# Performance work log

Measured on AMD Instinct MI355X. Metric: run time of the kernel, lower is better.

## Reference

```python
import math
import jax, jax.numpy as jnp
import numpy as np

SCALE = 4; K = 7; R = 3; K2 = K * K
BANDS = 10; FEAT = 64; HID = 256; HEADS = 4
LH = 96; LW = 96; H = LH * SCALE; W = LW * SCALE
IN_DIM = FEAT + 4 * BANDS + 2  # 106
REF_HID = 48  # 3 groups * 16


def _conv(x, w, b, groups=1):
    y = jax.lax.conv_general_dilated(x, w, (1, 1), 'SAME',
        dimension_numbers=('NCHW', 'OIHW', 'NCHW'), feature_group_count=groups)
    return y + b[None, :, None, None]


def _gelu(x):
    return jax.nn.gelu(x, approximate=False)  # torch nn.GELU default (erf)


def _gray(x):  # [B,3,H,W] -> [B,1,H,W]
    return 0.2989 * x[:, 0:1] + 0.587 * x[:, 1:2] + 0.114 * x[:, 2:3]


def setup_inputs() -> dict:
    key = jax.random.key(0)
    ks = iter(jax.random.split(key, 64))
    def W_(sh, s=0.05):
        return (jax.random.normal(next(ks), sh, dtype=jnp.float32) * s)
    def Z_(sh):
        return jnp.zeros(sh, jnp.float32)
    d = {}
    d['lr'] = jax.random.uniform(next(ks), (1, 3, LH, LW), dtype=jnp.float32)
    d['enc_w0'] = W_((FEAT, 3, 3, 3)); d['enc_b0'] = Z_((FEAT,))
    d['enc_w1'] = W_((FEAT, FEAT, 3, 3)); d['enc_b1'] = Z_((FEAT,))
    d['enc_w2'] = W_((FEAT, FEAT, 3, 3)); d['enc_b2'] = Z_((FEAT,))
    d['enc_w3'] = W_((FEAT, FEAT, 3, 3)); d['enc_b3'] = Z_((FEAT,))
    # cond_fuser: 1x1 convs, cond_ch=2 (hover bnd+mask, zeros at inference)
    d['cond_w0'] = W_((FEAT, FEAT + 2, 1, 1)); d['cond_b0'] = Z_((FEAT,))
    d['cond_w1'] = W_((FEAT, FEAT, 1, 1)); d['cond_b1'] = Z_((FEAT,))
    # KernelMLP backbone: 5 Linear layers
    d['mlp_w0'] = W_((IN_DIM, HID)); d['mlp_b0'] = Z_((HID,))
    d['mlp_w1'] = W_((HID, HID)); d['mlp_b1'] = Z_((HID,))
    d['mlp_w2'] = W_((HID, HID)); d['mlp_b2'] = Z_((HID,))
    d['mlp_w3'] = W_((HID, HID)); d['mlp_b3'] = Z_((HID,))
    d['mlp_w4'] = W_((HID, HID)); d['mlp_b4'] = Z_((HID,))
    d['hk_w'] = W_((HID, HEADS * K2)); d['hk_b'] = Z_((HEADS * K2,))
    d['hg_w'] = W_((HID, HEADS)); d['hg_b'] = Z_((HEADS,))
    # ResidualRefiner: grouped convs, groups=3 (OIHW with in/groups channels)
    d['ref_w0'] = W_((REF_HID, 2, 3, 3)); d['ref_b0'] = Z_((REF_HID,))
    d['ref_w1'] = W_((REF_HID, 16, 3, 3)); d['ref_b1'] = Z_((REF_HID,))
    d['ref_w2'] = W_((3, 16, 3, 3)); d['ref_b2'] = Z_((3,))
    return d


def reference(lr, enc_w0, enc_b0, enc_w1, enc_b1, enc_w2, enc_b2, enc_w3, enc_b3,
              cond_w0, cond_b0, cond_w1, cond_b1,
              mlp_w0, mlp_b0, mlp_w1, mlp_b1, mlp_w2, mlp_b2, mlp_w3, mlp_b3,
              mlp_w4, mlp_b4, hk_w, hk_b, hg_w, hg_b,
              ref_w0, ref_b0, ref_w1, ref_b1, ref_w2, ref_b2):
    # --- local CNN features on LR grid ---
    f = _gelu(_conv(lr, enc_w0, enc_b0))
    f = _gelu(_conv(f, enc_w1, enc_b1))
    f = _gelu(_conv(f, enc_w2, enc_b2))
    f = _gelu(_conv(f, enc_w3, enc_b3))
    cond = jnp.zeros((1, 2, LH, LW), f.dtype)  # no hover maps at inference
    f = _conv(jnp.concatenate([f, cond], axis=1), cond_w0, cond_b0)
    f = _conv(_gelu(f), cond_w1, cond_b1)
    # --- bilinear upsample (align_corners=False semantics) ---
    lr_up = jax.image.resize(lr, (1, 3, H, W), method='bilinear')
    # --- HR pixel grid -> LR centers + fractional offsets ---
    yy, xx = jnp.meshgrid(jnp.arange(H), jnp.arange(W), indexing='ij')
    xx = xx.reshape(-1).astype(jnp.float32)
    yy = yy.reshape(-1).astype(jnp.float32)
    lx = (xx + 0.5) / SCALE - 0.5
    ly = (yy + 0.5) / SCALE - 0.5
    cx = jnp.clip(jnp.round(lx), 0, LW - 1)
    cy = jnp.clip(jnp.round(ly), 0, LH - 1)
    dx = (lx - cx)[:, None]
    dy = (ly - cy)[:, None]
    cxi = cx.astype(jnp.int32)
    cyi = cy.astype(jnp.int32)
    idx = cyi * LW + cxi  # flattened gather index [N]
    feat_flat = f[0].reshape(FEAT, -1).T  # [lh*lw, FEAT]
    cf = feat_flat[idx]                   # [N, FEAT]
    # --- Fourier PE of normalized HR coords ---
    xn = (xx + 0.5) / W * 2.0 - 1.0
    yn = (yy + 0.5) / H * 2.0 - 1.0
    freq = (2.0 ** jnp.arange(BANDS, dtype=jnp.float32)) * math.pi
    ax = xn[:, None] * freq[None, :]
    ay = yn[:, None] * freq[None, :]
    pe = jnp.stack([jnp.sin(ax), jnp.cos(ax), jnp.sin(ay), jnp.cos(ay)], axis=-1)
    pe = pe.reshape(-1, 4 * BANDS)  # per-band [sinx,cosx,siny,cosy] order
    # --- per-pixel kernel MLP ---
    z = jnp.concatenate([cf, pe, dx, dy], axis=1)  # [N, 106]
    h = _gelu(z @ mlp_w0 + mlp_b0)
    h = _gelu(h @ mlp_w1 + mlp_b1)
    h = _gelu(h @ mlp_w2 + mlp_b2)
    h = _gelu(h @ mlp_w3 + mlp_b3)
    h = _gelu(h @ mlp_w4 + mlp_b4)
    klog = (h @ hk_w + hk_b).reshape(-1, HEADS, K2)
    glog = h @ hg_w + hg_b
    ker = jax.nn.softmax(klog, axis=-1)   # non-negative kernels
    gate = jax.nn.softmax(glog, axis=-1)  # head mixture
    kmix = jnp.einsum('nh,nhk->nk', gate, ker)  # [N, K2]
    # --- gather KxK LR neighborhood and apply adaptive kernel ---
    oy, ox = jnp.meshgrid(jnp.arange(-R, R + 1), jnp.arange(-R, R + 1), indexing='ij')
    ox = ox.reshape(-1); oy = oy.reshape(-1)  # offsets: oy outer, ox inner
    nx = jnp.clip(cxi[:, None] + ox[None, :], 0, LW - 1)
    ny = jnp.clip(cyi[:, None] + oy[None, :], 0, LH - 1)
    nidx = ny * LW + nx                     # [N, K2]
    lr_flat = lr[0].reshape(3, -1).T        # [lh*lw, 3]
    patches = lr_flat[nidx]                 # [N, K2, 3]
    pred = jnp.einsum('nk,nkc->nc', kmix, patches)  # [N, 3]
    sr = pred.reshape(H, W, 3).transpose(2, 0, 1)[None]  # [1,3,H,W]
    # --- color-safe residual refiner (groups=3) ---
    res0 = sr - lr_up
    x6 = jnp.concatenate([lr_up, res0], axis=1)
    r1 = _gelu(_conv(x6, ref_w0, ref_b0, groups=3))
    r1 = _gelu(_conv(r1, ref_w1, ref_b1, groups=3))
    res = _conv(r1, ref_w2, ref_b2, groups=3)
    sr2 = sr + res
    # --- color-preserving fusion: inject only grayscale residual ---
    delta = _gray(sr2) - _gray(lr_up)
    out = jnp.clip(lr_up + delta, 0.0, 1.0)
    return out
```

## Files before the change

### kernel.cpp

```cpp
#include <hip/hip_runtime.h>
#include <math.h>

#define LWI 96
#define LHI 96
#define HWD 384
#define NPIX 147456
#define LRPIX 9216
#define HID 256

typedef __attribute__((ext_vector_type(8))) _Float16 f16x8;
typedef __attribute__((ext_vector_type(4))) _Float16 f16x4;
typedef __attribute__((ext_vector_type(16))) float f32x16;

__device__ __forceinline__ float gelu_fast(float x){
  float x2 = x*x;
  float u = x*(-2.3021181f - 0.1029443f*x2);
  float e = exp2f(u);
  return x * __builtin_amdgcn_rcpf(1.0f + e);
}

__device__ __forceinline__ float lr_up_at(const float* __restrict__ lr, int c, int y, int x){
  float sy = (y+0.5f)*0.25f - 0.5f;
  float sx = (x+0.5f)*0.25f - 0.5f;
  float fy = floorf(sy), fx = floorf(sx);
  float ty = sy - fy, tx = sx - fx;
  int y0 = (int)fy, x0 = (int)fx;
  int y0c = min(max(y0,0),LHI-1), y1c = min(max(y0+1,0),LHI-1);
  int x0c = min(max(x0,0),LWI-1), x1c = min(max(x0+1,0),LWI-1);
  const float* p = lr + c*LRPIX;
  float v00 = p[y0c*LWI+x0c], v01 = p[y0c*LWI+x1c];
  float v10 = p[y1c*LWI+x0c], v11 = p[y1c*LWI+x1c];
  return (1.f-ty)*((1.f-tx)*v00 + tx*v01) + ty*((1.f-tx)*v10 + tx*v11);
}

__global__ __launch_bounds__(256) void conv3x3_f16out(
    const float* __restrict__ in, const float* __restrict__ w,
    const float* __restrict__ b, _Float16* __restrict__ out16){
  int tid = blockIdx.x*256 + threadIdx.x;
  int o = tid / LRPIX; int rem = tid - o*LRPIX;
  int y = rem / LWI;   int x = rem - y*LWI;
  int ou = __builtin_amdgcn_readfirstlane(o);
  float acc = b[ou];
  const float* wo = w + ou*27;
  for (int i=0;i<3;++i){
    const float* inp = in + i*LRPIX;
    #pragma unroll
    for (int dy=0;dy<3;++dy){
      int yy = y + dy - 1;
      bool yok = (yy>=0 && yy<LHI);
      #pragma unroll
      for (int dx=0;dx<3;++dx){
        int xx = x + dx - 1;
        float v = (yok && xx>=0 && xx<LWI) ? inp[yy*LWI+xx] : 0.0f;
        acc = fmaf(wo[i*9 + dy*3 + dx], v, acc);
      }
    }
  }
  out16[rem*64 + o] = (_Float16)gelu_fast(acc);
}

__global__ __launch_bounds__(256) void pack_convw(
  const float* __restrict__ cw1, const float* __restrict__ cw2,
  const float* __restrict__ cw3, const float* __restrict__ xw0,
  const float* __restrict__ xw1,
  _Float16* __restrict__ WC, _Float16* __restrict__ WX)
{
  int i = blockIdx.x*256 + threadIdx.x;
  if (i < 110592){
    int cv = i / 36864; int s2 = i - cv*36864;
    int tkf = s2 >> 9; int s = s2 & 511;
    int tap = tkf >> 3; int ksfb = tkf & 7;
    int ks = ksfb >> 1; int fb = ksfb & 1;
    int slot = s >> 3; int e = s & 7;
    int oc = fb*32 + (slot & 31);
    int ic = ks*16 + (slot>>5)*8 + e;
    int dy = tap/3, dx = tap - (tap/3)*3;
    const float* src = (cv==0)?cw1:(cv==1)?cw2:cw3;
    WC[i] = (_Float16)src[((oc*64+ic)*3+dy)*3+dx];
  } else if (i < 118784){
    int j = i - 110592;
    int cv = j >> 12; int s2 = j & 4095;
    int ks = s2 >> 10; int fb = (s2 >> 9) & 1; int s = s2 & 511;
    int slot = s >> 3; int e = s & 7;
    int oc = fb*32 + (slot & 31);
    int ic = ks*16 + (slot>>5)*8 + e;
    WX[j] = (_Float16)((cv==0) ? xw0[oc*66+ic] : xw1[oc*64+ic]);
  }
}

__global__ __launch_bounds__(256) void conv_mfma_kernel(
    const _Float16* __restrict__ Xin, const _Float16* __restrict__ WC,
    const float* __restrict__ bias, _Float16* __restrict__ Xout, int cv)
{
  __shared__ _Float16 xs[100*64];
  __shared__ float red[2][2][64][20];
  const int t = threadIdx.x;
  const int lane = t & 63;
  const int w = __builtin_amdgcn_readfirstlane(t >> 6);
  const int fb = w & 1, kh = w >> 1;
  const int g = lane >> 5;
  const int gx0 = blockIdx.x*8, gy0 = blockIdx.y*8;

  for (int i = t; i < 800; i += 256){
    int sp = i >> 3, c = i & 7;
    int ly = (sp*205)>>11; int lx = sp - ly*10;
    int gy = gy0 - 1 + ly, gx = gx0 - 1 + lx;
    f16x8 v = f16x8{};
    if (gy>=0 && gy<LHI && gx>=0 && gx<LWI)
      v = *(const f16x8*)(Xin + (gy*LWI+gx)*64 + c*8);
    *(f16x8*)(xs + sp*64 + ((c ^ (sp&7))*8)) = v;
  }
  __syncthreads();

  const _Float16* WCc = WC + cv*36864;
  const int p0 = lane & 31;
  const int py0 = p0 >> 3, px0 = p0 & 7;
  f32x16 acc0{}, acc1{};
  #pragma unroll
  for (int tap = 0; tap < 9; ++tap){
    const int dy = tap/3, dx = tap - (tap/3)*3;
    #pragma unroll
    for (int ksl = 0; ksl < 2; ++ksl){
      int ks = kh*2 + ksl;
      f16x8 A = *(const f16x8*)(WCc + ((tap*4+ks)*2+fb)*512 + lane*8);
      int sp0 = (py0+dy)*10 + (px0+dx);
      int sp1 = (py0+4+dy)*10 + (px0+dx);
      int c0 = ks*2 + g;
      f16x8 B0 = *(const f16x8*)(xs + sp0*64 + ((c0 ^ (sp0&7))*8));
      f16x8 B1 = *(const f16x8*)(xs + sp1*64 + ((c0 ^ (sp1&7))*8));
      acc0 = __builtin_amdgcn_mfma_f32_32x32x16_f16(A,B0,acc0,0,0,0);
      acc1 = __builtin_amdgcn_mfma_f32_32x32x16_f16(A,B1,acc1,0,0,0);
    }
  }
  if (kh == 1){
    #pragma unroll
    for (int r4=0;r4<4;++r4){
      float4 v0 = make_float4(acc0[r4*4],acc0[r4*4+1],acc0[r4*4+2],acc0[r4*4+3]);
      float4 v1 = make_float4(acc1[r4*4],acc1[r4*4+1],acc1[r4*4+2],acc1[r4*4+3]);
      *(float4*)&red[fb][0][lane][r4*4] = v0;
      *(float4*)&red[fb][1][lane][r4*4] = v1;
    }
  }
  __syncthreads();
  if (kh == 0){
    #pragma unroll
    for (int ph=0; ph<2; ++ph){
      const f32x16& acc = ph ? acc1 : acc0;
      int py = ph*4 + py0;
      int gpx = (gy0+py)*LWI + (gx0+px0);
      #pragma unroll
      for (int r4=0;r4<4;++r4){
        float4 rr = *(const float4*)&red[fb][ph][lane][r4*4];
        float4 bb = *(const float4*)&bias[fb*32 + 8*r4 + 4*g];
        f16x4 o;
        o[0] = (_Float16)gelu_fast(acc[r4*4+0] + rr.x + bb.x);
        o[1] = (_Float16)gelu_fast(acc[r4*4+1] + rr.y + bb.y);
        o[2] = (_Float16)gelu_fast(acc[r4*4+2] + rr.z + bb.z);
        o[3] = (_Float16)gelu_fast(acc[r4*4+3] + rr.w + bb.w);
        *(f16x4*)(Xout + gpx*64 + fb*32 + 8*r4 + 4*g) = o;
      }
    }
  }
}

__global__ __launch_bounds__(256) void conv1x1_mfma(
    const _Float16* __restrict__ Xin, const _Float16* __restrict__ W1,
    const float* __restrict__ bias, _Float16* __restrict__ Xout, int dogelu)
{
  __shared__ _Float16 bufB[4096];
  const int t = threadIdx.x;
  const int lane = t & 63;
  const int w = __builtin_amdgcn_readfirstlane(t >> 6);
  const int fb = w & 1, ph = w >> 1;
  const int px0 = blockIdx.x * 64;
  #pragma unroll
  for (int h = 0; h < 2; ++h){
    int i = t + h*256;
    int p = i & 63, c = i >> 6;
    f16x8 v = *(const f16x8*)(Xin + (px0+p)*64 + c*8);
    *(f16x8*)(bufB + ((c>>1)*2 + (p>>5))*512 + ((p&31)+32*(c&1))*8) = v;
  }
  __syncthreads();
  f32x16 acc{};
  #pragma unroll
  for (int ks=0; ks<4; ++ks){
    f16x8 A = *(const f16x8*)(W1 + (ks*2+fb)*512 + lane*8);
    f16x8 B = *(const f16x8*)(bufB + (ks*2+ph)*512 + lane*8);
    acc = __builtin_amdgcn_mfma_f32_32x32x16_f16(A,B,acc,0,0,0);
  }
  const int p31 = lane & 31, hi = lane >> 5;
  int px = px0 + ph*32 + p31;
  #pragma unroll
  for (int q=0;q<4;++q){
    float4 bb = *(const float4*)&bias[fb*32 + q*8 + 4*hi];
    const float* bp = (const float*)&bb;
    f16x4 o;
    #pragma unroll
    for (int r=0;r<4;++r){
      float v = acc[q*4+r] + bp[r];
      o[r] = (_Float16)(dogelu ? gelu_fast(v) : v);
    }
    *(f16x4*)(Xout + px*64 + fb*32 + q*8 + 4*hi) = o;
  }
}

__global__ __launch_bounds__(256) void pack_weights(
  const float* __restrict__ mw0, const float* __restrict__ mw1,
  const float* __restrict__ mw2, const float* __restrict__ mw3,
  const float* __restrict__ mw4, const float* __restrict__ hkw,
  const float* __restrict__ hgw,
  const float* __restrict__ mb0, const float* __restrict__ mb1,
  const float* __restrict__ mb2, const float* __restrict__ mb3,
  const float* __restrict__ mb4, const float* __restrict__ hkb,
  const float* __restrict__ hgb,
  _Float16* __restrict__ WB, float* __restrict__ biasAll)
{
  int i = blockIdx.x*256 + threadIdx.x;
  if (i < 356352){
    int layer, local;
    if (i < 28672){ layer = 0; local = i; }
    else { layer = 1 + ((i-28672)>>16); local = (i-28672)&65535; }
    int ks = local >> 12; int r = local & 4095;
    int cb = r >> 9; int s2 = r & 511; int slot = s2 >> 3; int e = s2 & 7;
    int col = cb*32 + (slot & 31); int g = slot >> 5;
    int k = ks*16 + g*8 + e;
    float v = 0.f;
    if (layer == 0){ if (k < 106) v = mw0[k*256+col]; }
    else if (layer == 1) v = mw1[k*256+col];
    else if (layer == 2) v = mw2[k*256+col];
    else if (layer == 3) v = mw3[k*256+col];
    else if (layer == 4) v = mw4[k*256+col];
    else { if (col < 196) v = hkw[k*196+col]; else if (col < 200) v = hgw[k*4+col-196]; }
    WB[i] = (_Float16)v;
  } else if (i < 356352+1536){
    int j = i - 356352; int layer = j>>8; int col = j&255;
    float v = 0.f;
    if (layer==0) v=mb0[col]; else if (layer==1) v=mb1[col]; else if(layer==2) v=mb2[col];
    else if(layer==3) v=mb3[col]; else if(layer==4) v=mb4[col];
    else { if (col<196) v=hkb[col]; else if(col<200) v=hgb[col-196]; }
    biasAll[j] = v;
  }
}

template<int NKS>
__device__ __forceinline__ void mlp_pass(const _Float16* __restrict__ Wl,
    const _Float16* __restrict__ buf, int lane, int w, f32x16 (&acc)[2]){
  acc[0] = f32x16{}; acc[1] = f32x16{};
  #pragma unroll
  for (int ks=0; ks<NKS; ++ks){
    f16x8 a = *(const f16x8*)(Wl + (ks*8+w)*512 + lane*8);
    const _Float16* bp = buf + ks*1024 + lane*8;
    f16x8 b0 = *(const f16x8*)(bp);
    f16x8 b1 = *(const f16x8*)(bp + 512);
    acc[0] = __builtin_amdgcn_mfma_f32_32x32x16_f16(a,b0,acc[0],0,0,0);
    acc[1] = __builtin_amdgcn_mfma_f32_32x32x16_f16(a,b1,acc[1],0,0,0);
  }
}

__global__ __launch_bounds__(512,6) void mlp_mfma3_kernel(
  const _Float16* __restrict__ feat16, const float* __restrict__ lr,
  const _Float16* __restrict__ WB, const float* __restrict__ biasAll,
  float* __restrict__ sr)
{
  __shared__ _Float16 buf[16384];
  const int t = threadIdx.x;
  const int lane = t & 63;
  const int w = __builtin_amdgcn_readfirstlane(t >> 6);
  const int p31 = lane & 31; const int hi = lane >> 5;

  {
    const int p = lane; const int q = w;
    const int px = blockIdx.x*64 + p;
    const int y = px / HWD; const int x = px - y*HWD;
    float lx = (x+0.5f)*0.25f - 0.5f;
    float ly = (y+0.5f)*0.25f - 0.5f;
    float cxf = fminf(fmaxf(rintf(lx),0.f),95.f);
    float cyf = fminf(fmaxf(rintf(ly),0.f),95.f);
    int base = (int)cyf*LWI + (int)cxf;
    auto zwrite = [&](int k, float v){
      buf[((k>>4)*2 + (p>>5))*512 + ((p&31) + 32*((k>>3)&1))*8 + (k&7)] = (_Float16)v;
    };
    auto zwriteh = [&](int k, _Float16 v){
      buf[((k>>4)*2 + (p>>5))*512 + ((p&31) + 32*((k>>3)&1))*8 + (k&7)] = v;
    };
    if (q < 2){
      const _Float16* fsrc = feat16 + base*64 + q*32;
      #pragma unroll
      for (int j=0;j<32;++j) zwriteh(q*32+j, fsrc[j]);
    } else if (q == 2){
      float xn = (x+0.5f)/384.0f*2.0f - 1.0f;
      float s = sinf(xn*3.14159265358979323846f);
      float c = cosf(xn*3.14159265358979323846f);
      #pragma unroll
      for (int b=0;b<10;++b){
        zwrite(64+4*b+0, s); zwrite(64+4*b+1, c);
        float s2 = 2.f*s*c; float c2 = 1.f - 2.f*s*s;
        s=s2; c=c2;
      }
      zwrite(104, lx-cxf); zwrite(105, ly-cyf);
    } else if (q == 3){
      float yn = (y+0.5f)/384.0f*2.0f - 1.0f;
      float s = sinf(yn*3.14159265358979323846f);
      float c = cosf(yn*3.14159265358979323846f);
      #pragma unroll
      for (int b=0;b<10;++b){
        zwrite(64+4*b+2, s); zwrite(64+4*b+3, c);
        float s2 = 2.f*s*c; float c2 = 1.f - 2.f*s*s;
        s=s2; c=c2;
      }
    } else if (q == 4){
      #pragma unroll
      for (int k=106;k<112;++k) zwrite(k, 0.f);
    }
  }
  __syncthreads();

  #pragma unroll 1
  for (int L=0; L<5; ++L){
    static const int WOFFS[5] = {0,28672,94208,159744,225280};
    f32x16 acc[2];
    if (L==0) mlp_pass<7>(WB, buf, lane, w, acc);
    else      mlp_pass<16>(WB + WOFFS[L], buf, lane, w, acc);
    __syncthreads();
    const float* Bl = biasAll + L*256;
    #pragma unroll
    for (int q2=0;q2<4;++q2){
      float4 bs = *(const float4*)&Bl[w*32 + q2*8 + 4*hi];
      const float* bp2 = (const float*)&bs;
      int ks2 = w*2 + (q2>>1); int g2 = q2&1;
      _Float16* dst = buf + (ks2*2)*512 + (p31 + 32*g2)*8 + 4*hi;
      #pragma unroll
      for (int pb=0;pb<2;++pb){
        f16x4 o;
        #pragma unroll
        for (int r=0;r<4;++r) o[r] = (_Float16)gelu_fast(acc[pb][q2*4+r] + bp2[r]);
        *(f16x4*)(dst + pb*512) = o;
      }
    }
    __syncthreads();
  }

  {
    f32x16 acc[2];
    if (w < 7) mlp_pass<16>(WB + 290816, buf, lane, w, acc);
    __syncthreads();
    if (w < 7){
      #pragma unroll
      for (int reg=0;reg<16;++reg){
        int f = w*32 + (reg&3) + 8*(reg>>2) + 4*hi;
        if (f < 200){
          float bias = biasAll[1280 + f];
          buf[f*72 + p31]      = (_Float16)(acc[0][reg] + bias);
          buf[f*72 + 32 + p31] = (_Float16)(acc[1][reg] + bias);
        }
      }
    }
  }
  __syncthreads();

  if (t < 256){
    const int p = t & 63; const int hd = t >> 6;
    auto KL = [&](int col)->float { return (float)buf[col*72 + p]; };
    const float L2E = 1.4426950408889634f;
    float g0=KL(196),g1=KL(197),g2=KL(198),g3=KL(199);
    float gm = fmaxf(fmaxf(g0,g1),fmaxf(g2,g3));
    float e0=exp2f((g0-gm)*L2E),e1=exp2f((g1-gm)*L2E),
          e2=exp2f((g2-gm)*L2E),e3=exp2f((g3-gm)*L2E);
    float gate = ((hd==0)?e0:(hd==1)?e1:(hd==2)?e2:e3)/(e0+e1+e2+e3);
    float m = -1e30f;
    #pragma unroll
    for (int k=0;k<49;++k) m = fmaxf(m, KL(hd*49+k));
    float s = 0.f;
    float ev[49];
    #pragma unroll
    for (int k=0;k<49;++k){ float e=exp2f((KL(hd*49+k)-m)*L2E); s+=e; ev[k]=e; }
    float sc = gate/s;
    #pragma unroll
    for (int k=0;k<49;++k) buf[(hd*49+k)*72 + p] = (_Float16)(ev[k]*sc);
  }
  __syncthreads();

  {
    float kv[7];
    #pragma unroll
    for (int j=0;j<7;++j){
      int i = t + j*512;
      if (i < 3136){
        int k = i >> 6, p = i & 63;
        kv[j] = (float)buf[k*72+p] + (float)buf[(49+k)*72+p]
              + (float)buf[(98+k)*72+p] + (float)buf[(147+k)*72+p];
      }
    }
    __syncthreads();
    #pragma unroll
    for (int j=0;j<7;++j){
      int i = t + j*512;
      if (i < 3136){
        int k = i >> 6, p = i & 63;
        buf[k*72+p] = (_Float16)kv[j];
      }
    }
  }
  __syncthreads();

  if (t < 192){
    const int c = t >> 6; const int p = t & 63;
    const int px = blockIdx.x*64 + p;
    const int y = px / HWD; const int x = px - y*HWD;
    float lx = (x+0.5f)*0.25f - 0.5f;
    float ly = (y+0.5f)*0.25f - 0.5f;
    int cxi = (int)fminf(fmaxf(rintf(lx),0.f),95.f);
    int cyi = (int)fminf(fmaxf(rintf(ly),0.f),95.f);
    const float* lrc = lr + c*LRPIX;
    float acc = 0.f;
    bool interior = (cxi>=3 && cxi<=92 && cyi>=3 && cyi<=92);
    if (__all(interior)){
      const float* lrb = lrc + (cyi-3)*LWI + (cxi-3);
      #pragma unroll
      for (int k=0;k<49;++k){
        float km = (float)buf[k*72+p];
        acc = fmaf(km, lrb[(k/7)*LWI + (k - (k/7)*7)], acc);
      }
    } else {
      #pragma unroll
      for (int k=0;k<49;++k){
        float km = (float)buf[k*72+p];
        int oy = k/7 - 3, ox = k - (k/7)*7 - 3;
        int nyy = min(max(cyi+oy,0),95), nxx = min(max(cxi+ox,0),95);
        acc = fmaf(km, lrc[nyy*LWI+nxx], acc);
      }
    }
    sr[c*NPIX + px] = acc;
  }
}

__global__ __launch_bounds__(256) void refiner_group_kernel(
  const float* __restrict__ lr, const float* __restrict__ srg,
  const float* __restrict__ w0, const float* __restrict__ b0,
  const float* __restrict__ w1, const float* __restrict__ b1,
  const float* __restrict__ w2, const float* __restrict__ b2,
  float* __restrict__ resW)
{
  __shared__ float x6s[2][22][26];
  __shared__ float r1a[16][20][20];
  __shared__ float r1b[16][18][20];
  const int g = blockIdx.z;
  const int tid = threadIdx.x;
  const int gx0 = blockIdx.x*16, gy0 = blockIdx.y*16;

  for (int i = tid; i < 2*22*22; i += 256){
    int ic = i / 484; int rem = i - ic*484; int yy = rem / 22; int xx = rem - yy*22;
    int ch = g*2 + ic;
    int gy = gy0 - 3 + yy, gx = gx0 - 3 + xx;
    float v = 0.f;
    if (gy>=0 && gy<HWD && gx>=0 && gx<HWD){
      int c = (ch<3)?ch:(ch-3);
      float lu = lr_up_at(lr, c, gy, gx);
      v = (ch < 3) ? lu : (srg[c*NPIX + gy*HWD + gx] - lu);
    }
    x6s[ic][yy][xx] = v;
  }
  __syncthreads();

  for (int task = tid; task < 320; task += 256){
    int o = task / 20; int yy = task - o*20;
    int og = g*16 + o;
    float bias = b0[og];
    float acc[20];
    #pragma unroll
    for (int j=0;j<20;++j) acc[j] = bias;
    #pragma unroll
    for (int ic=0; ic<2; ++ic){
      #pragma unroll
      for (int dyy=0; dyy<3; ++dyy){
        float row[22];
        #pragma unroll
        for (int j=0;j<22;++j) row[j] = x6s[ic][yy+dyy][j];
        #pragma unroll
        for (int dxx=0; dxx<3; ++dxx){
          float wv = w0[((og*2+ic)*3+dyy)*3+dxx];
          #pragma unroll
          for (int j=0;j<20;++j) acc[j] = fmaf(wv, row[j+dxx], acc[j]);
        }
      }
    }
    int gyy = gy0 - 2 + yy;
    bool rok = (gyy>=0 && gyy<HWD);
    #pragma unroll
    for (int j=0;j<20;++j){
      int gxx = gx0 - 2 + j;
      r1a[o][yy][j] = (rok && gxx>=0 && gxx<HWD) ? gelu_fast(acc[j]) : 0.f;
    }
  }
  __syncthreads();

  for (int task = tid; task < 288; task += 256){
    int o = task / 18; int yy = task - o*18;
    int og = g*16 + o;
    float bias = b1[og];
    float acc[18];
    #pragma unroll
    for (int j=0;j<18;++j) acc[j] = bias;
    for (int ic=0; ic<16; ++ic){
      #pragma unroll
      for (int dyy=0; dyy<3; ++dyy){
        float row[20];
        #pragma unroll
        for (int q=0;q<5;++q)
          *(float4*)&row[q*4] = *(const float4*)&r1a[ic][yy+dyy][q*4];
        #pragma unroll
        for (int dxx=0; dxx<3; ++dxx){
          float wv = w1[((og*16+ic)*3+dyy)*3+dxx];
          #pragma unroll
          for (int j=0;j<18;++j) acc[j] = fmaf(wv, row[j+dxx], acc[j]);
        }
      }
    }
    int gyy = gy0 - 1 + yy;
    bool rok = (gyy>=0 && gyy<HWD);
    #pragma unroll
    for (int j=0;j<18;++j){
      int gxx = gx0 - 1 + j;
      r1b[o][yy][j] = (rok && gxx>=0 && gxx<HWD) ? gelu_fast(acc[j]) : 0.f;
    }
  }
  __syncthreads();

  {
    int ty = tid >> 4, tx = tid & 15;
    float a = b2[g];
    for (int ic=0; ic<16; ++ic){
      #pragma unroll
      for (int dyy=0; dyy<3; ++dyy){
        #pragma unroll
        for (int dxx=0; dxx<3; ++dxx){
          a = fmaf(w2[((g*16+ic)*3+dyy)*3+dxx], r1b[ic][ty+dyy][tx+dxx], a);
        }
      }
    }
    resW[g*NPIX + (gy0+ty)*HWD + gx0+tx] = a;
  }
}

__global__ __launch_bounds__(256) void fuse_kernel(
  const float* __restrict__ lr, const float* __restrict__ srg,
  const float* __restrict__ resW, float* __restrict__ out)
{
  int p = blockIdx.x*256 + threadIdx.x;
  int y = p / HWD, x = p - y*HWD;
  float lu[3];
  float d = 0.f;
  const float cf0=0.2989f, cf1=0.587f, cf2=0.114f;
  lu[0] = lr_up_at(lr, 0, y, x);
  lu[1] = lr_up_at(lr, 1, y, x);
  lu[2] = lr_up_at(lr, 2, y, x);
  d += cf0*(srg[0*NPIX+p] + resW[0*NPIX+p] - lu[0]);
  d += cf1*(srg[1*NPIX+p] + resW[1*NPIX+p] - lu[1]);
  d += cf2*(srg[2*NPIX+p] + resW[2*NPIX+p] - lu[2]);
  #pragma unroll
  for (int c=0;c<3;++c){
    float o_ = lu[c] + d;
    out[c*NPIX + p] = fminf(fmaxf(o_, 0.f), 1.f);
  }
}

extern "C" void kernel_launch(void* const* d_in, const int* in_sizes, int n_in,
                              void* d_out, int out_size, void* d_ws, size_t ws_size,
                              hipStream_t stream){
  const float* lr  = (const float*)d_in[0];
  const float* ew0 = (const float*)d_in[1];  const float* eb0 = (const float*)d_in[2];
  const float* ew1 = (const float*)d_in[3];  const float* eb1 = (const float*)d_in[4];
  const float* ew2 = (const float*)d_in[5];  const float* eb2 = (const float*)d_in[6];
  const float* ew3 = (const float*)d_in[7];  const float* eb3 = (const float*)d_in[8];
  const float* cw0 = (const float*)d_in[9];  const float* cb0 = (const float*)d_in[10];
  const float* cw1 = (const float*)d_in[11]; const float* cb1 = (const float*)d_in[12];
  const float* mw0 = (const float*)d_in[13]; const float* mb0 = (const float*)d_in[14];
  const float* mw1 = (const float*)d_in[15]; const float* mb1 = (const float*)d_in[16];
  const float* mw2 = (const float*)d_in[17]; const float* mb2 = (const float*)d_in[18];
  const float* mw3 = (const float*)d_in[19]; const float* mb3 = (const float*)d_in[20];
  const float* mw4 = (const float*)d_in[21]; const float* mb4 = (const float*)d_in[22];
  const float* hkw = (const float*)d_in[23]; const float* hkb = (const float*)d_in[24];
  const float* hgw = (const float*)d_in[25]; const float* hgb = (const float*)d_in[26];
  const float* rw0 = (const float*)d_in[27]; const float* rb0 = (const float*)d_in[28];
  const float* rw1 = (const float*)d_in[29]; const float* rb1 = (const float*)d_in[30];
  const float* rw2 = (const float*)d_in[31]; const float* rb2 = (const float*)d_in[32];

  float* ws = (float*)d_ws;
  _Float16* X0 = (_Float16*)ws;
  _Float16* X1 = (_Float16*)(ws + 294912);
  float* srp   = ws + 589824;
  _Float16* WB = (_Float16*)(ws + 1032192);
  _Float16* WC = (_Float16*)(ws + 1210368);
  float* biasAll = ws + 1265664;
  float* resW  = ws + 1267200;
  _Float16* WX = (_Float16*)(ws + 1709568);

  pack_weights<<<1398,256,0,stream>>>(mw0,mw1,mw2,mw3,mw4,hkw,hgw,
      mb0,mb1,mb2,mb3,mb4,hkb,hgb, WB, biasAll);
  pack_convw<<<464,256,0,stream>>>(ew1, ew2, ew3, cw0, cw1, WC, WX);

  conv3x3_f16out<<<2304,256,0,stream>>>(lr, ew0, eb0, X0);
  conv_mfma_kernel<<<dim3(12,12),256,0,stream>>>(X0, WC, eb1, X1, 0);
  conv_mfma_kernel<<<dim3(12,12),256,0,stream>>>(X1, WC, eb2, X0, 1);
  conv_mfma_kernel<<<dim3(12,12),256,0,stream>>>(X0, WC, eb3, X1, 2);
  conv1x1_mfma<<<144,256,0,stream>>>(X1, WX,        cb0, X0, 1);
  conv1x1_mfma<<<144,256,0,stream>>>(X0, WX + 4096, cb1, X1, 0);

  mlp_mfma3_kernel<<<2304,512,0,stream>>>(X1, lr, WB, biasAll, srp);

  refiner_group_kernel<<<dim3(24,24,3),256,0,stream>>>(lr, srp,
      rw0,rb0, rw1,rb1, rw2,rb2, resW);
  fuse_kernel<<<576,256,0,stream>>>(lr, srp, resW, (float*)d_out);
}
```

Baseline: 324.0 us.

## Halve MLP block to 4 waves, each computing 64 output features

The MLP kernel drops from 8 waves (512 threads) to 4 waves (256 threads) per 64-pixel block. Each wave now computes a 64-feature slice with four MFMA accumulators, so every activation B-fragment loaded from shared memory feeds two MFMAs. The feature-setup, softmax and kernel-sum phases are reassigned to fit 256 threads. This trades higher register pressure and fewer waves for latency hiding against less LDS traffic and fewer barrier participants.

New measurement: 324.8 us. About the same (+0.2%).

```diff
diff --git a/kernel.cpp b/kernel.cpp
--- a/kernel.cpp
+++ b/kernel.cpp
@@ -243,21 +243,25 @@
 }
 
 template<int NKS>
-__device__ __forceinline__ void mlp_pass(const _Float16* __restrict__ Wl,
-    const _Float16* __restrict__ buf, int lane, int w, f32x16 (&acc)[2]){
-  acc[0] = f32x16{}; acc[1] = f32x16{};
+__device__ __forceinline__ void mlp_pass4(const _Float16* __restrict__ Wl,
+    const _Float16* __restrict__ buf, int lane, int w, f32x16 (&acc)[4]){
+  acc[0]=f32x16{}; acc[1]=f32x16{}; acc[2]=f32x16{}; acc[3]=f32x16{};
   #pragma unroll
   for (int ks=0; ks<NKS; ++ks){
-    f16x8 a = *(const f16x8*)(Wl + (ks*8+w)*512 + lane*8);
+    const _Float16* wp = Wl + (ks*8 + 2*w)*512 + lane*8;
+    f16x8 a0 = *(const f16x8*)(wp);
+    f16x8 a1 = *(const f16x8*)(wp + 512);
     const _Float16* bp = buf + ks*1024 + lane*8;
     f16x8 b0 = *(const f16x8*)(bp);
     f16x8 b1 = *(const f16x8*)(bp + 512);
-    acc[0] = __builtin_amdgcn_mfma_f32_32x32x16_f16(a,b0,acc[0],0,0,0);
-    acc[1] = __builtin_amdgcn_mfma_f32_32x32x16_f16(a,b1,acc[1],0,0,0);
-  }
-}
-
-__global__ __launch_bounds__(512,6) void mlp_mfma3_kernel(
+    acc[0] = __builtin_amdgcn_mfma_f32_32x32x16_f16(a0,b0,acc[0],0,0,0);
+    acc[1] = __builtin_amdgcn_mfma_f32_32x32x16_f16(a0,b1,acc[1],0,0,0);
+    acc[2] = __builtin_amdgcn_mfma_f32_32x32x16_f16(a1,b0,acc[2],0,0,0);
+    acc[3] = __builtin_amdgcn_mfma_f32_32x32x16_f16(a1,b1,acc[3],0,0,0);
+  }
+}
+
+__global__ __launch_bounds__(256,4) void mlp_mfma7_kernel(
   const _Float16* __restrict__ feat16, const float* __restrict__ lr,
   const _Float16* __restrict__ WB, const float* __restrict__ biasAll,
   float* __restrict__ sr)
@@ -298,7 +302,7 @@
         s=s2; c=c2;
       }
       zwrite(104, lx-cxf); zwrite(105, ly-cyf);
-    } else if (q == 3){
+    } else {
       float yn = (y+0.5f)/384.0f*2.0f - 1.0f;
       float s = sinf(yn*3.14159265358979323846f);
       float c = cosf(yn*3.14159265358979323846f);
@@ -308,7 +312,6 @@
         float s2 = 2.f*s*c; float c2 = 1.f - 2.f*s*s;
         s=s2; c=c2;
       }
-    } else if (q == 4){
       #pragma unroll
       for (int k=106;k<112;++k) zwrite(k, 0.f);
     }
@@ -318,47 +321,54 @@
   #pragma unroll 1
   for (int L=0; L<5; ++L){
     static const int WOFFS[5] = {0,28672,94208,159744,225280};
-    f32x16 acc[2];
-    if (L==0) mlp_pass<7>(WB, buf, lane, w, acc);
-    else      mlp_pass<16>(WB + WOFFS[L], buf, lane, w, acc);
+    f32x16 acc[4];
+    if (L==0) mlp_pass4<7>(WB, buf, lane, w, acc);
+    else      mlp_pass4<16>(WB + WOFFS[L], buf, lane, w, acc);
     __syncthreads();
     const float* Bl = biasAll + L*256;
     #pragma unroll
-    for (int q2=0;q2<4;++q2){
-      float4 bs = *(const float4*)&Bl[w*32 + q2*8 + 4*hi];
-      const float* bp2 = (const float*)&bs;
-      int ks2 = w*2 + (q2>>1); int g2 = q2&1;
-      _Float16* dst = buf + (ks2*2)*512 + (p31 + 32*g2)*8 + 4*hi;
-      #pragma unroll
-      for (int pb=0;pb<2;++pb){
-        f16x4 o;
+    for (int i=0;i<2;++i){
+      const int F = w*64 + i*32;
+      #pragma unroll
+      for (int q2=0;q2<4;++q2){
+        float4 bs = *(const float4*)&Bl[F + q2*8 + 4*hi];
+        const float* bp2 = (const float*)&bs;
+        int ks2 = (F>>4) + (q2>>1); int g2 = q2&1;
+        _Float16* dst = buf + (ks2*2)*512 + (p31 + 32*g2)*8 + 4*hi;
         #pragma unroll
-        for (int r=0;r<4;++r) o[r] = (_Float16)gelu_fast(acc[pb][q2*4+r] + bp2[r]);
-        *(f16x4*)(dst + pb*512) = o;
+        for (int pb=0;pb<2;++pb){
+          const f32x16& a = acc[i*2+pb];
+          f16x4 o;
+          #pragma unroll
+          for (int r=0;r<4;++r) o[r] = (_Float16)gelu_fast(a[q2*4+r] + bp2[r]);
+          *(f16x4*)(dst + pb*512) = o;
+        }
       }
     }
     __syncthreads();
   }
 
   {
-    f32x16 acc[2];
-    if (w < 7) mlp_pass<16>(WB + 290816, buf, lane, w, acc);
+    f32x16 acc[4];
+    mlp_pass4<16>(WB + 290816, buf, lane, w, acc);
     __syncthreads();
-    if (w < 7){
+    #pragma unroll
+    for (int i=0;i<2;++i){
+      const int F = w*64 + i*32;
       #pragma unroll
       for (int reg=0;reg<16;++reg){
-        int f = w*32 + (reg&3) + 8*(reg>>2) + 4*hi;
+        int f = F + (reg&3) + 8*(reg>>2) + 4*hi;
         if (f < 200){
           float bias = biasAll[1280 + f];
-          buf[f*72 + p31]      = (_Float16)(acc[0][reg] + bias);
-          buf[f*72 + 32 + p31] = (_Float16)(acc[1][reg] + bias);
+          buf[f*72 + p31]      = (_Float16)(acc[i*2+0][reg] + bias);
+          buf[f*72 + 32 + p31] = (_Float16)(acc[i*2+1][reg] + bias);
         }
       }
     }
   }
   __syncthreads();
 
-  if (t < 256){
+  {
     const int p = t & 63; const int hd = t >> 6;
     auto KL = [&](int col)->float { return (float)buf[col*72 + p]; };
     const float L2E = 1.4426950408889634f;
@@ -381,10 +391,10 @@
   __syncthreads();
 
   {
-    float kv[7];
-    #pragma unroll
-    for (int j=0;j<7;++j){
-      int i = t + j*512;
+    float kv[13];
+    #pragma unroll
+    for (int j=0;j<13;++j){
+      int i = t + j*256;
       if (i < 3136){
         int k = i >> 6, p = i & 63;
         kv[j] = (float)buf[k*72+p] + (float)buf[(49+k)*72+p]
@@ -393,8 +403,8 @@
     }
     __syncthreads();
     #pragma unroll
-    for (int j=0;j<7;++j){
-      int i = t + j*512;
+    for (int j=0;j<13;++j){
+      int i = t + j*256;
       if (i < 3136){
         int k = i >> 6, p = i & 63;
         buf[k*72+p] = (_Float16)kv[j];
@@ -606,7 +616,7 @@
   conv1x1_mfma<<<144,256,0,stream>>>(X1, WX,        cb0, X0, 1);
   conv1x1_mfma<<<144,256,0,stream>>>(X0, WX + 4096, cb1, X1, 0);
 
-  mlp_mfma3_kernel<<<2304,512,0,stream>>>(X1, lr, WB, biasAll, srp);
+  mlp_mfma7_kernel<<<2304,256,0,stream>>>(X1, lr, WB, biasAll, srp);
 
   refiner_group_kernel<<<dim3(24,24,3),256,0,stream>>>(lr, srp,
       rw0,rb0, rw1,rb1, rw2,rb2, resW);
```
